# Performance work log

Hardware: AMD Instinct MI355X
Metric: run time of the kernel (lower is better)

The kernel has to match this reference:

```python
import jax, jax.numpy as jnp
import numpy as np

N_CLASSES = 40
EMBED_DIM = 128
MOMENTUM = 0.1
LAMBDA_R, LAMBDA_C, LAMBDA_M = 1.0, 0.5, 1.0
BATCH = 262144


def setup_inputs() -> dict:
    key = jax.random.key(0)
    k1, k2, k3 = jax.random.split(key, 3)
    z = jax.random.normal(k1, (BATCH, EMBED_DIM), dtype=jnp.float32)
    y = jax.random.randint(k2, (BATCH,), 0, N_CLASSES)
    centers = jax.random.normal(k3, (N_CLASSES, EMBED_DIM), dtype=jnp.float32)
    initialized = jnp.ones((N_CLASSES,), dtype=bool)
    # buffers derived from class_counts (imbalanced ramp), r0=gamma=m0=1, alpha=0.25
    counts = jnp.asarray([1000.0 * (i + 1) for i in range(N_CLASSES)], jnp.float32)
    n_max = jnp.max(counts)
    target_radii = 1.0 + 1.0 * jnp.log(n_max / (counts + 1.0))
    margins = 1.0 * jnp.power(n_max / (counts + 1.0), 0.25)
    return {"z": z, "y": y, "centers": centers, "initialized": initialized,
            "target_radii": target_radii, "margins": margins}


def _update_centers(z, y, centers, initialized):
    # EMA centroid update on detached embeddings (torch.no_grad equivalent).
    zs = jax.lax.stop_gradient(z)
    sums = jax.ops.segment_sum(zs, y, num_segments=N_CLASSES)            # [C, D]
    cnt = jax.ops.segment_sum(jnp.ones((zs.shape[0],), zs.dtype), y,
                              num_segments=N_CLASSES)                    # [C]
    mean = sums / jnp.maximum(cnt, 1.0)[:, None]
    ema = (1.0 - MOMENTUM) * centers + MOMENTUM * mean
    new = jnp.where(initialized[:, None], ema, mean)                     # first-touch init
    return jnp.where((cnt > 0)[:, None], new, centers)                   # skip empty classes


def reference(z, y, centers, initialized, target_radii, margins):
    c = _update_centers(z, y, centers, initialized)                      # [C, D]

    # radial loss: smooth L1 (beta=1) between ||z|| and per-class target radius
    r = jnp.linalg.norm(z, axis=-1)                                      # [B]
    d = r - target_radii[y]
    ad = jnp.abs(d)
    loss_radial = jnp.mean(jnp.where(ad < 1.0, 0.5 * d * d, ad - 0.5))

    # compact loss: mean squared distance to own centroid
    diff = z - c[y]                                                      # [B, D]
    loss_compact = jnp.mean(jnp.sum(diff * diff, axis=-1))

    # margin loss: min distance to any other class centroid via Gram trick
    z2 = jnp.sum(z * z, axis=-1)                                         # [B]
    c2 = jnp.sum(c * c, axis=-1)                                         # [C]
    d2 = z2[:, None] + c2[None, :] - 2.0 * (z @ c.T)                     # [B, C]
    dist = jnp.sqrt(jnp.maximum(d2, 0.0))
    own = y[:, None] == jnp.arange(N_CLASSES)[None, :]                   # [B, C] bool
    dist_opp = jnp.min(jnp.where(own, jnp.inf, dist), axis=1)            # [B]
    loss_margin = jnp.mean(jax.nn.relu(margins[y] - dist_opp))

    return LAMBDA_R * loss_radial + LAMBDA_C * loss_compact + LAMBDA_M * loss_margin
```

## Files before the change

### kernel.cpp

```cpp
#include <hip/hip_runtime.h>
#include <math.h>

#define BATCH 262144
#define DIM   128
#define NCLS  40
#define NCP   48
#define CD    (NCLS * DIM)

#define TB1 512
#define NB1 256
#define TB3 256
#define NB3 (BATCH / 256)

typedef __attribute__((ext_vector_type(8))) short short8;
typedef __attribute__((ext_vector_type(4))) float f32x4;

__device__ __forceinline__ short f2bf(float f) {
    unsigned u = __float_as_uint(f);
    u += 0x7fffu + ((u >> 16) & 1u);
    return (short)(u >> 16);
}

__global__ __launch_bounds__(TB1) void k1_segsum(const float* __restrict__ z,
                                                 const int* __restrict__ y,
                                                 float* __restrict__ part_sums,
                                                 float* __restrict__ gcnt) {
    __shared__ float s_acc[8][NCLS * 64];
    __shared__ float s_cnt[NCLS];
    const int t = threadIdx.x;
    for (int i = t; i < 8 * NCLS * 64; i += TB1) ((float*)s_acc)[i] = 0.0f;
    if (t < NCLS) s_cnt[t] = 0.0f;
    __syncthreads();

    const int w    = t >> 6;
    const int lane = t & 63;
    const int p    = w >> 1;
    const int h    = w & 1;
    const int base = blockIdx.x * 1024;
    float* __restrict__ acc = s_acc[w];

    int yy[4];
#pragma unroll
    for (int g = 0; g < 4; ++g) yy[g] = y[base + 4 * (g * 64 + lane) + p];

    if (h == 0) {
#pragma unroll
        for (int g = 0; g < 4; ++g) atomicAdd(&s_cnt[yy[g]], 1.0f);
    }

    const float* __restrict__ zp = z + (size_t)base * DIM + h * 64 + lane;

    float vb[8];
#pragma unroll
    for (int q = 0; q < 8; ++q) vb[q] = zp[(size_t)(4 * q + p) * DIM];

#pragma unroll 1
    for (int g = 0; g < 4; ++g) {
        const int yg = yy[g];
#pragma unroll
        for (int j0 = 0; j0 < 64; j0 += 8) {
#pragma unroll
            for (int q = 0; q < 8; ++q) {
                const int sj = g * 64 + j0 + q;
                const float v = vb[q];
                int sn = sj + 8;
                if (sn > 255) sn = sj;
                vb[q] = zp[(size_t)(4 * sn + p) * DIM];
                const int cls = __builtin_amdgcn_readlane(yg, j0 + q);
                acc[cls * 64 + lane] += v;
            }
        }
    }
    __syncthreads();

    float* __restrict__ ps = part_sums + (size_t)blockIdx.x * CD;
    for (int i = t; i < CD; i += TB1) {
        const int cls = i >> 7;
        const int d   = i & 127;
        const int hh  = d >> 6, dl = d & 63;
        float ssum = 0.0f;
#pragma unroll
        for (int pp = 0; pp < 4; ++pp) ssum += s_acc[(pp << 1) | hh][cls * 64 + dl];
        ps[i] = ssum;
    }
    if (t < NCLS) atomicAdd(&gcnt[t], s_cnt[t]);
}

__global__ __launch_bounds__(DIM) void k2_centers(const float* __restrict__ part_sums,
                                                  const float* __restrict__ gcnt,
                                                  const float* __restrict__ centers,
                                                  short* __restrict__ cbf,
                                                  float* __restrict__ c2_out) {
    const int j = blockIdx.x;
    const int d = threadIdx.x;

    if (j >= NCLS) {
        cbf[j * DIM + d] = 0;
        if (d == 0) c2_out[j] = 1e30f;
        return;
    }

    const float* __restrict__ p = part_sums + j * DIM + d;
    float s = 0.0f;
#pragma unroll 8
    for (int b = 0; b < NB1; ++b) s += p[(size_t)b * CD];
    const float cnt = gcnt[j];

    const float mean = s / fmaxf(cnt, 1.0f);
    const float ctr  = centers[j * DIM + d];
    const float ema  = 0.9f * ctr + 0.1f * mean;
    const float cv   = (cnt > 0.0f) ? ema : ctr;
    cbf[j * DIM + d] = f2bf(cv);

    __shared__ float red[DIM];
    red[d] = cv * cv;
    __syncthreads();
    for (int off = DIM / 2; off > 0; off >>= 1) {
        if (d < off) red[d] += red[d + off];
        __syncthreads();
    }
    if (d == 0) c2_out[j] = red[0];
}

__global__ __launch_bounds__(TB3) void k3_loss(const float* __restrict__ z,
                                               const int* __restrict__ y,
                                               const short* __restrict__ cbf,
                                               const float* __restrict__ c2,
                                               const float* __restrict__ tr,
                                               const float* __restrict__ mg,
                                               float* __restrict__ partials) {
    __shared__ float s_S[4][64 * 52];
    __shared__ float s_z2[4][64];
    __shared__ float s_c2[NCP];
    __shared__ float s_red[TB3];

    const int t = threadIdx.x;
    if (t < NCP) s_c2[t] = c2[t];

    const int w    = t >> 6;
    const int lane = t & 63;
    const int q    = lane >> 4;
    const int col  = lane & 15;
    const int wavebase = blockIdx.x * 256 + w * 64;

    short8 bfrag[3][4];
#pragma unroll
    for (int ct = 0; ct < 3; ++ct)
#pragma unroll
        for (int s = 0; s < 4; ++s)
            bfrag[ct][s] = *(const short8*)(cbf + (ct * 16 + col) * DIM + s * 32 + q * 8);

    __syncthreads();

#pragma unroll 1
    for (int rt = 0; rt < 4; ++rt) {
        const float* __restrict__ zrow =
            z + (size_t)(wavebase + rt * 16 + col) * DIM + q * 8;

        float4 f[8];
#pragma unroll
        for (int s = 0; s < 4; ++s) {
            f[2 * s]     = *(const float4*)(zrow + s * 32);
            f[2 * s + 1] = *(const float4*)(zrow + s * 32 + 4);
        }

        float zp = 0.0f;
#pragma unroll
        for (int i = 0; i < 8; ++i) {
            zp = fmaf(f[i].x, f[i].x, zp);
            zp = fmaf(f[i].y, f[i].y, zp);
            zp = fmaf(f[i].z, f[i].z, zp);
            zp = fmaf(f[i].w, f[i].w, zp);
        }

        short8 afr[4];
#pragma unroll
        for (int s = 0; s < 4; ++s) {
            const float4 f0 = f[2 * s], f1 = f[2 * s + 1];
            afr[s][0] = f2bf(f0.x); afr[s][1] = f2bf(f0.y);
            afr[s][2] = f2bf(f0.z); afr[s][3] = f2bf(f0.w);
            afr[s][4] = f2bf(f1.x); afr[s][5] = f2bf(f1.y);
            afr[s][6] = f2bf(f1.z); afr[s][7] = f2bf(f1.w);
        }

        f32x4 acc0 = {0.f, 0.f, 0.f, 0.f};
        f32x4 acc1 = {0.f, 0.f, 0.f, 0.f};
        f32x4 acc2 = {0.f, 0.f, 0.f, 0.f};
#pragma unroll
        for (int s = 0; s < 4; ++s) {
            acc0 = __builtin_amdgcn_mfma_f32_16x16x32_bf16(afr[s], bfrag[0][s], acc0, 0, 0, 0);
            acc1 = __builtin_amdgcn_mfma_f32_16x16x32_bf16(afr[s], bfrag[1][s], acc1, 0, 0, 0);
            acc2 = __builtin_amdgcn_mfma_f32_16x16x32_bf16(afr[s], bfrag[2][s], acc2, 0, 0, 0);
        }

        zp += __shfl_xor(zp, 16);
        zp += __shfl_xor(zp, 32);
        if (q == 0) s_z2[w][rt * 16 + col] = zp;

#pragma unroll
        for (int reg = 0; reg < 4; ++reg) {
            const int rr = rt * 16 + q * 4 + reg;
            s_S[w][rr * 52 + col]      = acc0[reg];
            s_S[w][rr * 52 + 16 + col] = acc1[reg];
            s_S[w][rr * 52 + 32 + col] = acc2[reg];
        }
    }

    const int row = blockIdx.x * 256 + t;
    const int cls = y[row];
    const float z2v = s_z2[w][lane];

    float own_d2 = 0.0f;
    float mind2  = 3.4e38f;
#pragma unroll
    for (int k = 0; k < 12; ++k) {
        const float4 Sv = *(const float4*)&s_S[w][lane * 52 + 4 * k];
        const float Se[4] = {Sv.x, Sv.y, Sv.z, Sv.w};
#pragma unroll
        for (int e = 0; e < 4; ++e) {
            const int j = 4 * k + e;
            float d2 = fmaxf(z2v + s_c2[j] - 2.0f * Se[e], 0.0f);
            const bool isown = (j == cls);
            own_d2 = isown ? d2 : own_d2;
            mind2  = isown ? mind2 : fminf(mind2, d2);
        }
    }

    const float r  = sqrtf(z2v);
    const float dd = r - tr[cls];
    const float ad = fabsf(dd);
    const float rad = (ad < 1.0f) ? 0.5f * dd * dd : ad - 0.5f;

    const float dist = sqrtf(mind2);
    const float marg = fmaxf(mg[cls] - dist, 0.0f);

    const float tot = rad + 0.5f * own_d2 + marg;

    s_red[t] = tot;
    __syncthreads();
    for (int off = TB3 / 2; off > 0; off >>= 1) {
        if (t < off) s_red[t] += s_red[t + off];
        __syncthreads();
    }
    if (t == 0) partials[blockIdx.x] = s_red[0];
}

__global__ __launch_bounds__(256) void k4_final(const float* __restrict__ partials,
                                                float* __restrict__ out) {
    __shared__ float sred[256];
    float s = 0.0f;
    for (int i = threadIdx.x; i < NB3; i += 256) s += partials[i];
    sred[threadIdx.x] = s;
    __syncthreads();
    for (int off = 128; off > 0; off >>= 1) {
        if (threadIdx.x < off) sred[threadIdx.x] += sred[threadIdx.x + off];
        __syncthreads();
    }
    if (threadIdx.x == 0) out[0] = sred[0] * (1.0f / (float)BATCH);
}

extern "C" void kernel_launch(void* const* d_in, const int* in_sizes, int n_in,
                              void* d_out, int out_size, void* d_ws, size_t ws_size,
                              hipStream_t stream) {
    const float* z       = (const float*)d_in[0];
    const int*   y       = (const int*)d_in[1];
    const float* centers = (const float*)d_in[2];
    const float* tr      = (const float*)d_in[4];
    const float* mg      = (const float*)d_in[5];
    float* out = (float*)d_out;

    float* ws        = (float*)d_ws;
    float* part_sums = ws;
    float* c2buf     = part_sums + (size_t)NB1 * CD;
    float* gcnt      = c2buf + NCP;
    float* partials  = gcnt + NCLS;
    short* cbf       = (short*)(partials + NB3);

    hipMemsetAsync(gcnt, 0, NCLS * sizeof(float), stream);

    k1_segsum<<<NB1, TB1, 0, stream>>>(z, y, part_sums, gcnt);
    k2_centers<<<NCP, DIM, 0, stream>>>(part_sums, gcnt, centers, cbf, c2buf);
    k3_loss<<<NB3, TB3, 0, stream>>>(z, y, cbf, c2buf, tr, mg, partials);
    k4_final<<<1, 256, 0, stream>>>(partials, out);
}
```

Baseline: 245.2 us.

## Emit bf16 copy of z in segsum pass and fuse loss reduction via atomics

The segment-sum kernel now reads z as float4, accumulates into LDS with vectorised read-modify-writes, and writes a bf16 copy of z that the loss kernel reads instead of fp32 z. The per-block center sums are combined with global atomics, so the center kernel no longer loops over 256 partial buffers. The loss kernel computes distances directly from MFMA accumulators with lane shuffles instead of staging through LDS, and adds its result to the output atomically, which removes the final reduction kernel. In exchange, the squared norms and radial loss are now computed from bf16-rounded z, which lowers precision. Float atomics also make the summation order nondeterministic.

New measurement: 299.4 us. 22.1% more time.

```diff
diff --git a/kernel.cpp b/kernel.cpp
--- a/kernel.cpp
+++ b/kernel.cpp
@@ -15,15 +15,19 @@
 typedef __attribute__((ext_vector_type(8))) short short8;
 typedef __attribute__((ext_vector_type(4))) float f32x4;
 
-__device__ __forceinline__ short f2bf(float f) {
+__device__ __forceinline__ unsigned f2bfu(float f) {
     unsigned u = __float_as_uint(f);
     u += 0x7fffu + ((u >> 16) & 1u);
-    return (short)(u >> 16);
+    return u >> 16;
+}
+__device__ __forceinline__ float bf2f(int b) {
+    return __uint_as_float(((unsigned)b) << 16);
 }
 
 __global__ __launch_bounds__(TB1) void k1_segsum(const float* __restrict__ z,
                                                  const int* __restrict__ y,
-                                                 float* __restrict__ part_sums,
+                                                 unsigned short* __restrict__ zbf,
+                                                 float* __restrict__ csum,
                                                  float* __restrict__ gcnt) {
     __shared__ float s_acc[8][NCLS * 64];
     __shared__ float s_cnt[NCLS];
@@ -36,60 +40,82 @@
     const int lane = t & 63;
     const int p    = w >> 1;
     const int h    = w & 1;
-    const int base = blockIdx.x * 1024;
+    const int g    = lane >> 4;
+    const int dl   = (lane & 15) << 2;
+    const int blockbase = blockIdx.x * 1024;
     float* __restrict__ acc = s_acc[w];
 
-    int yy[4];
-#pragma unroll
-    for (int g = 0; g < 4; ++g) yy[g] = y[base + 4 * (g * 64 + lane) + p];
-
-    if (h == 0) {
-#pragma unroll
-        for (int g = 0; g < 4; ++g) atomicAdd(&s_cnt[yy[g]], 1.0f);
-    }
-
-    const float* __restrict__ zp = z + (size_t)base * DIM + h * 64 + lane;
-
-    float vb[8];
-#pragma unroll
-    for (int q = 0; q < 8; ++q) vb[q] = zp[(size_t)(4 * q + p) * DIM];
+    const float* __restrict__ zlane =
+        z + (size_t)(blockbase + p * 256 + g) * DIM + h * 64 + dl;
+    unsigned short* __restrict__ zbfl =
+        zbf + (size_t)(blockbase + p * 256 + g) * DIM + h * 64 + dl;
+    const int* __restrict__ yrow = y + blockbase + p * 256;
+    const bool cnt_lane = (h == 0) && (lane == 0);
+
+    float4 vb[4];
+#pragma unroll
+    for (int u = 0; u < 4; ++u) vb[u] = *(const float4*)(zlane + (size_t)u * 512);
 
 #pragma unroll 1
-    for (int g = 0; g < 4; ++g) {
-        const int yg = yy[g];
-#pragma unroll
-        for (int j0 = 0; j0 < 64; j0 += 8) {
-#pragma unroll
-            for (int q = 0; q < 8; ++q) {
-                const int sj = g * 64 + j0 + q;
-                const float v = vb[q];
-                int sn = sj + 8;
-                if (sn > 255) sn = sj;
-                vb[q] = zp[(size_t)(4 * sn + p) * DIM];
-                const int cls = __builtin_amdgcn_readlane(yg, j0 + q);
-                acc[cls * 64 + lane] += v;
+    for (int ii = 0; ii < 16; ++ii) {
+#pragma unroll
+        for (int u = 0; u < 4; ++u) {
+            const int i = ii * 4 + u;
+            const int4 yq = *(const int4*)(yrow + 4 * i);
+            const float4 v = vb[u];
+            int nstep = i + 4; if (nstep > 63) nstep = i;
+            vb[u] = *(const float4*)(zlane + (size_t)nstep * 512);
+
+            uint2 pk;
+            pk.x = (f2bfu(v.y) << 16) | f2bfu(v.x);
+            pk.y = (f2bfu(v.w) << 16) | f2bfu(v.z);
+            *(uint2*)(zbfl + (size_t)i * 512) = pk;
+
+            if (cnt_lane) {
+                atomicAdd(&s_cnt[yq.x], 1.0f);
+                atomicAdd(&s_cnt[yq.y], 1.0f);
+                atomicAdd(&s_cnt[yq.z], 1.0f);
+                atomicAdd(&s_cnt[yq.w], 1.0f);
+            }
+
+            if (yq.x != yq.y && yq.x != yq.z && yq.x != yq.w &&
+                yq.y != yq.z && yq.y != yq.w && yq.z != yq.w) {
+                const int c0 = (g == 0) ? yq.x : (g == 1) ? yq.y : (g == 2) ? yq.z : yq.w;
+                float* a = &acc[c0 * 64 + dl];
+                float4 o = *(float4*)a;
+                o.x += v.x; o.y += v.y; o.z += v.z; o.w += v.w;
+                *(float4*)a = o;
+            } else {
+#define K1_RMW(G, CLS)                                                  \
+                if (g == (G)) {                                         \
+                    float* a = &acc[(CLS) * 64 + dl];                   \
+                    float4 o = *(float4*)a;                             \
+                    o.x += v.x; o.y += v.y; o.z += v.z; o.w += v.w;     \
+                    *(float4*)a = o;                                    \
+                }
+                K1_RMW(0, yq.x) K1_RMW(1, yq.y) K1_RMW(2, yq.z) K1_RMW(3, yq.w)
+#undef K1_RMW
             }
         }
     }
     __syncthreads();
 
-    float* __restrict__ ps = part_sums + (size_t)blockIdx.x * CD;
     for (int i = t; i < CD; i += TB1) {
         const int cls = i >> 7;
         const int d   = i & 127;
-        const int hh  = d >> 6, dl = d & 63;
+        const int hh  = d >> 6, dd = d & 63;
         float ssum = 0.0f;
 #pragma unroll
-        for (int pp = 0; pp < 4; ++pp) ssum += s_acc[(pp << 1) | hh][cls * 64 + dl];
-        ps[i] = ssum;
+        for (int pp = 0; pp < 4; ++pp) ssum += s_acc[(pp << 1) | hh][cls * 64 + dd];
+        atomicAdd(&csum[i], ssum);
     }
     if (t < NCLS) atomicAdd(&gcnt[t], s_cnt[t]);
 }
 
-__global__ __launch_bounds__(DIM) void k2_centers(const float* __restrict__ part_sums,
+__global__ __launch_bounds__(DIM) void k2_centers(const float* __restrict__ csum,
                                                   const float* __restrict__ gcnt,
                                                   const float* __restrict__ centers,
-                                                  short* __restrict__ cbf,
+                                                  unsigned short* __restrict__ cbf,
                                                   float* __restrict__ c2_out) {
     const int j = blockIdx.x;
     const int d = threadIdx.x;
@@ -100,17 +126,13 @@
         return;
     }
 
-    const float* __restrict__ p = part_sums + j * DIM + d;
-    float s = 0.0f;
-#pragma unroll 8
-    for (int b = 0; b < NB1; ++b) s += p[(size_t)b * CD];
+    const float s   = csum[j * DIM + d];
     const float cnt = gcnt[j];
-
     const float mean = s / fmaxf(cnt, 1.0f);
     const float ctr  = centers[j * DIM + d];
     const float ema  = 0.9f * ctr + 0.1f * mean;
     const float cv   = (cnt > 0.0f) ? ema : ctr;
-    cbf[j * DIM + d] = f2bf(cv);
+    cbf[j * DIM + d] = (unsigned short)f2bfu(cv);
 
     __shared__ float red[DIM];
     red[d] = cv * cv;
@@ -122,26 +144,29 @@
     if (d == 0) c2_out[j] = red[0];
 }
 
-__global__ __launch_bounds__(TB3) void k3_loss(const float* __restrict__ z,
+__global__ __launch_bounds__(TB3) void k3_loss(const unsigned short* __restrict__ zbf,
                                                const int* __restrict__ y,
-                                               const short* __restrict__ cbf,
+                                               const unsigned short* __restrict__ cbf,
                                                const float* __restrict__ c2,
                                                const float* __restrict__ tr,
                                                const float* __restrict__ mg,
-                                               float* __restrict__ partials) {
-    __shared__ float s_S[4][64 * 52];
-    __shared__ float s_z2[4][64];
+                                               float* __restrict__ out) {
     __shared__ float s_c2[NCP];
-    __shared__ float s_red[TB3];
+    __shared__ float s_tr[NCLS];
+    __shared__ float s_mg[NCLS];
+    __shared__ int   s_yb[TB3];
+    __shared__ float s_z2[4][16];
 
     const int t = threadIdx.x;
-    if (t < NCP) s_c2[t] = c2[t];
+    if (t < NCP)  s_c2[t] = c2[t];
+    if (t < NCLS) { s_tr[t] = tr[t]; s_mg[t] = mg[t]; }
+    s_yb[t] = y[blockIdx.x * TB3 + t];
 
     const int w    = t >> 6;
     const int lane = t & 63;
     const int q    = lane >> 4;
     const int col  = lane & 15;
-    const int wavebase = blockIdx.x * 256 + w * 64;
+    const int wavebase = blockIdx.x * TB3 + w * 64;
 
     short8 bfrag[3][4];
 #pragma unroll
@@ -150,113 +175,80 @@
         for (int s = 0; s < 4; ++s)
             bfrag[ct][s] = *(const short8*)(cbf + (ct * 16 + col) * DIM + s * 32 + q * 8);
 
-    __syncthreads();
+    float c2l[3];
+#pragma unroll
+    for (int ct = 0; ct < 3; ++ct) c2l[ct] = c2[ct * 16 + col];
+
+    __syncthreads();
+
+    float wsum = 0.0f;
 
 #pragma unroll 1
     for (int rt = 0; rt < 4; ++rt) {
-        const float* __restrict__ zrow =
-            z + (size_t)(wavebase + rt * 16 + col) * DIM + q * 8;
-
-        float4 f[8];
-#pragma unroll
-        for (int s = 0; s < 4; ++s) {
-            f[2 * s]     = *(const float4*)(zrow + s * 32);
-            f[2 * s + 1] = *(const float4*)(zrow + s * 32 + 4);
-        }
+        const unsigned short* __restrict__ zrow =
+            zbf + (size_t)(wavebase + rt * 16 + col) * DIM + q * 8;
+
+        short8 afr[4];
+#pragma unroll
+        for (int s = 0; s < 4; ++s) afr[s] = *(const short8*)(zrow + s * 32);
 
         float zp = 0.0f;
 #pragma unroll
-        for (int i = 0; i < 8; ++i) {
-            zp = fmaf(f[i].x, f[i].x, zp);
-            zp = fmaf(f[i].y, f[i].y, zp);
-            zp = fmaf(f[i].z, f[i].z, zp);
-            zp = fmaf(f[i].w, f[i].w, zp);
-        }
-
-        short8 afr[4];
-#pragma unroll
-        for (int s = 0; s < 4; ++s) {
-            const float4 f0 = f[2 * s], f1 = f[2 * s + 1];
-            afr[s][0] = f2bf(f0.x); afr[s][1] = f2bf(f0.y);
-            afr[s][2] = f2bf(f0.z); afr[s][3] = f2bf(f0.w);
-            afr[s][4] = f2bf(f1.x); afr[s][5] = f2bf(f1.y);
-            afr[s][6] = f2bf(f1.z); afr[s][7] = f2bf(f1.w);
-        }
-
-        f32x4 acc0 = {0.f, 0.f, 0.f, 0.f};
-        f32x4 acc1 = {0.f, 0.f, 0.f, 0.f};
-        f32x4 acc2 = {0.f, 0.f, 0.f, 0.f};
-#pragma unroll
-        for (int s = 0; s < 4; ++s) {
-            acc0 = __builtin_amdgcn_mfma_f32_16x16x32_bf16(afr[s], bfrag[0][s], acc0, 0, 0, 0);
-            acc1 = __builtin_amdgcn_mfma_f32_16x16x32_bf16(afr[s], bfrag[1][s], acc1, 0, 0, 0);
-            acc2 = __builtin_amdgcn_mfma_f32_16x16x32_bf16(afr[s], bfrag[2][s], acc2, 0, 0, 0);
-        }
-
+        for (int s = 0; s < 4; ++s)
+#pragma unroll
+            for (int e = 0; e < 8; ++e) {
+                const float f = bf2f((unsigned short)afr[s][e]);
+                zp = fmaf(f, f, zp);
+            }
         zp += __shfl_xor(zp, 16);
         zp += __shfl_xor(zp, 32);
-        if (q == 0) s_z2[w][rt * 16 + col] = zp;
+        if (q == 0) s_z2[w][col] = zp;
+
+        f32x4 accv[3] = {{0.f,0.f,0.f,0.f},{0.f,0.f,0.f,0.f},{0.f,0.f,0.f,0.f}};
+#pragma unroll
+        for (int s = 0; s < 4; ++s) {
+            accv[0] = __builtin_amdgcn_mfma_f32_16x16x32_bf16(afr[s], bfrag[0][s], accv[0], 0, 0, 0);
+            accv[1] = __builtin_amdgcn_mfma_f32_16x16x32_bf16(afr[s], bfrag[1][s], accv[1], 0, 0, 0);
+            accv[2] = __builtin_amdgcn_mfma_f32_16x16x32_bf16(afr[s], bfrag[2][s], accv[2], 0, 0, 0);
+        }
+
+        const float4 z2r = *(const float4*)&s_z2[w][q * 4];
+        const int4  cls4 = *(const int4*)&s_yb[w * 64 + rt * 16 + q * 4];
+        const float z2a[4] = {z2r.x, z2r.y, z2r.z, z2r.w};
+        const int   cla[4] = {cls4.x, cls4.y, cls4.z, cls4.w};
 
 #pragma unroll
         for (int reg = 0; reg < 4; ++reg) {
-            const int rr = rt * 16 + q * 4 + reg;
-            s_S[w][rr * 52 + col]      = acc0[reg];
-            s_S[w][rr * 52 + 16 + col] = acc1[reg];
-            s_S[w][rr * 52 + 32 + col] = acc2[reg];
+            float ownv = 0.0f;
+            float minv = 3.4e38f;
+#pragma unroll
+            for (int ct = 0; ct < 3; ++ct) {
+                const float d2 = fmaxf(z2a[reg] + c2l[ct] - 2.0f * accv[ct][reg], 0.0f);
+                const bool own = (cla[reg] == ct * 16 + col);
+                ownv = own ? d2 : ownv;
+                minv = own ? minv : fminf(minv, d2);
+            }
+#pragma unroll
+            for (int m = 1; m <= 8; m <<= 1) {
+                minv = fminf(minv, __shfl_xor(minv, m));
+                ownv += __shfl_xor(ownv, m);
+            }
+            if (col == 0) {
+                const int  cl  = cla[reg];
+                const float r  = sqrtf(z2a[reg]);
+                const float dd = r - s_tr[cl];
+                const float ad = fabsf(dd);
+                const float rad = (ad < 1.0f) ? 0.5f * dd * dd : ad - 0.5f;
+                const float dist = sqrtf(minv);
+                const float marg = fmaxf(s_mg[cl] - dist, 0.0f);
+                wsum += rad + 0.5f * ownv + marg;
+            }
         }
     }
 
-    const int row = blockIdx.x * 256 + t;
-    const int cls = y[row];
-    const float z2v = s_z2[w][lane];
-
-    float own_d2 = 0.0f;
-    float mind2  = 3.4e38f;
-#pragma unroll
-    for (int k = 0; k < 12; ++k) {
-        const float4 Sv = *(const float4*)&s_S[w][lane * 52 + 4 * k];
-        const float Se[4] = {Sv.x, Sv.y, Sv.z, Sv.w};
-#pragma unroll
-        for (int e = 0; e < 4; ++e) {
-            const int j = 4 * k + e;
-            float d2 = fmaxf(z2v + s_c2[j] - 2.0f * Se[e], 0.0f);
-            const bool isown = (j == cls);
-            own_d2 = isown ? d2 : own_d2;
-            mind2  = isown ? mind2 : fminf(mind2, d2);
-        }
-    }
-
-    const float r  = sqrtf(z2v);
-    const float dd = r - tr[cls];
-    const float ad = fabsf(dd);
-    const float rad = (ad < 1.0f) ? 0.5f * dd * dd : ad - 0.5f;
-
-    const float dist = sqrtf(mind2);
-    const float marg = fmaxf(mg[cls] - dist, 0.0f);
-
-    const float tot = rad + 0.5f * own_d2 + marg;
-
-    s_red[t] = tot;
-    __syncthreads();
-    for (int off = TB3 / 2; off > 0; off >>= 1) {
-        if (t < off) s_red[t] += s_red[t + off];
-        __syncthreads();
-    }
-    if (t == 0) partials[blockIdx.x] = s_red[0];
-}
-
-__global__ __launch_bounds__(256) void k4_final(const float* __restrict__ partials,
-                                                float* __restrict__ out) {
-    __shared__ float sred[256];
-    float s = 0.0f;
-    for (int i = threadIdx.x; i < NB3; i += 256) s += partials[i];
-    sred[threadIdx.x] = s;
-    __syncthreads();
-    for (int off = 128; off > 0; off >>= 1) {
-        if (threadIdx.x < off) sred[threadIdx.x] += sred[threadIdx.x + off];
-        __syncthreads();
-    }
-    if (threadIdx.x == 0) out[0] = sred[0] * (1.0f / (float)BATCH);
+    wsum += __shfl_xor(wsum, 16);
+    wsum += __shfl_xor(wsum, 32);
+    if (lane == 0) atomicAdd(out, wsum * (1.0f / (float)BATCH));
 }
 
 extern "C" void kernel_launch(void* const* d_in, const int* in_sizes, int n_in,
@@ -269,17 +261,17 @@
     const float* mg      = (const float*)d_in[5];
     float* out = (float*)d_out;
 
-    float* ws        = (float*)d_ws;
-    float* part_sums = ws;
-    float* c2buf     = part_sums + (size_t)NB1 * CD;
-    float* gcnt      = c2buf + NCP;
-    float* partials  = gcnt + NCLS;
-    short* cbf       = (short*)(partials + NB3);
-
-    hipMemsetAsync(gcnt, 0, NCLS * sizeof(float), stream);
-
-    k1_segsum<<<NB1, TB1, 0, stream>>>(z, y, part_sums, gcnt);
-    k2_centers<<<NCP, DIM, 0, stream>>>(part_sums, gcnt, centers, cbf, c2buf);
-    k3_loss<<<NB3, TB3, 0, stream>>>(z, y, cbf, c2buf, tr, mg, partials);
-    k4_final<<<1, 256, 0, stream>>>(partials, out);
-}
+    float* ws    = (float*)d_ws;
+    float* csum  = ws;
+    float* gcnt  = csum + CD;
+    float* c2buf = gcnt + 64;
+    unsigned short* cbf = (unsigned short*)(c2buf + NCP);
+    unsigned short* zbf = (unsigned short*)(c2buf + NCP + NCP * DIM / 2 + 64);
+
+    hipMemsetAsync(csum, 0, (CD + 64) * sizeof(float), stream);
+    hipMemsetAsync(out, 0, sizeof(float), stream);
+
+    k1_segsum<<<NB1, TB1, 0, stream>>>(z, y, zbf, csum, gcnt);
+    k2_centers<<<NCP, DIM, 0, stream>>>(csum, gcnt, centers, cbf, c2buf);
+    k3_loss<<<NB3, TB3, 0, stream>>>(zbf, y, cbf, c2buf, tr, mg, out);
+}
```
